# Kernel tuning notes

Measured on AMD Instinct MI355X. Metric: run time of the kernel, lower is better.

Reference implementation:

```python
import math
import jax, jax.numpy as jnp
import numpy as np

B, D, C = 1024, 512, 100000
S = 30.0
M = 0.3
COS_M = math.cos(M)
SIN_M = math.sin(M)
TH = math.cos(math.pi - M)
MM = math.sin(math.pi - M) * M
EPS = 1e-12  # torch F.normalize eps


def _l2norm(x):
    n = jnp.sqrt(jnp.sum(x * x, axis=-1, keepdims=True))
    return x / jnp.maximum(n, EPS)


def setup_inputs() -> dict:
    key = jax.random.key(0)
    k1, k2, k3 = jax.random.split(key, 3)
    features = jax.random.normal(k1, (B, D), dtype=jnp.float32)
    # xavier_uniform_ for weight [C, D]
    limit = math.sqrt(6.0 / (C + D))
    weight = jax.random.uniform(k2, (C, D), dtype=jnp.float32, minval=-limit, maxval=limit)
    targets = jax.random.randint(k3, (B,), 0, C, dtype=jnp.int64)
    return {"features": features, "weight": weight, "targets": targets}


def reference(features, weight, targets):
    # cosine similarity via normalized GEMM: [B, C]
    cosine = _l2norm(features) @ _l2norm(weight).T
    cosine = cosine.astype(jnp.float32)
    sine = jnp.sqrt(jnp.maximum(1.0 - cosine * cosine, 0.0))
    phi = cosine * COS_M - sine * SIN_M
    # easy_margin=False branch
    phi = jnp.where(cosine > TH, phi, cosine - MM)
    # one-hot blend (ls_eps == 0): target column gets phi, rest keep cosine
    one_hot = targets[:, None] == jnp.arange(C)[None, :]
    logits = jnp.where(one_hot, phi, cosine) * S
    # CrossEntropyLoss (mean reduction)
    logp = jax.nn.log_softmax(logits, axis=-1)
    loss = -jnp.mean(jnp.take_along_axis(logp, targets[:, None], axis=1))
    return loss
```

## Files before the change

### kernel.cpp

```cpp
#include <hip/hip_runtime.h>

#define B_ROWS 1024
#define D_DIM  512
#define C_CLS  100000
#define N_TILES 782
#define GRID_NJ 98

typedef unsigned short u16;
typedef __attribute__((ext_vector_type(8))) short bf16x8;
typedef __attribute__((ext_vector_type(4))) float f32x4;

__device__ __forceinline__ u16 f2bf(float f) {
  unsigned u = __float_as_uint(f);
  u += 0x7fffu + ((u >> 16) & 1u);
  return (u16)(u >> 16);
}

__device__ __forceinline__ bf16x8 pack8(float4 a, float4 b) {
  union { bf16x8 v; unsigned u[4]; } r;
  r.u[0] = __builtin_amdgcn_perm(__float_as_uint(a.y), __float_as_uint(a.x), 0x07060302u);
  r.u[1] = __builtin_amdgcn_perm(__float_as_uint(a.w), __float_as_uint(a.z), 0x07060302u);
  r.u[2] = __builtin_amdgcn_perm(__float_as_uint(b.y), __float_as_uint(b.x), 0x07060302u);
  r.u[3] = __builtin_amdgcn_perm(__float_as_uint(b.w), __float_as_uint(b.z), 0x07060302u);
  return r.v;
}

__device__ __forceinline__ void gll16(const void* g, void* l) {
  __builtin_amdgcn_global_load_lds(
      (const __attribute__((address_space(1))) unsigned int*)g,
      (__attribute__((address_space(3))) unsigned int*)l, 16, 0, 0);
}

__global__ void norm_feat_kernel(const float* __restrict__ in, u16* __restrict__ out)
{
  const int row  = blockIdx.x * 4 + (threadIdx.x >> 6);
  const int lane = threadIdx.x & 63;
  const float4* r = (const float4*)(in + (size_t)row * D_DIM);
  float4 v0 = r[lane];
  float4 v1 = r[lane + 64];
  float ss = v0.x*v0.x + v0.y*v0.y + v0.z*v0.z + v0.w*v0.w
           + v1.x*v1.x + v1.y*v1.y + v1.z*v1.z + v1.w*v1.w;
#pragma unroll
  for (int m = 1; m < 64; m <<= 1) ss += __shfl_xor(ss, m);
  const float inv = 1.0f / fmaxf(sqrtf(ss), 1e-12f);
  ushort4 o0, o1;
  o0.x = f2bf(v0.x * inv); o0.y = f2bf(v0.y * inv);
  o0.z = f2bf(v0.z * inv); o0.w = f2bf(v0.w * inv);
  o1.x = f2bf(v1.x * inv); o1.y = f2bf(v1.y * inv);
  o1.z = f2bf(v1.z * inv); o1.w = f2bf(v1.w * inv);
  ushort4* orow = (ushort4*)(out + (size_t)row * D_DIM);
  orow[lane]      = o0;
  orow[lane + 64] = o1;
}

__global__ __launch_bounds__(256, 4) void arc_gemm(
    const u16* __restrict__ fn, const float* __restrict__ wt,
    const int* __restrict__ targets, float* __restrict__ psum,
    float* __restrict__ tlogit)
{
  __shared__ u16 As[128 * 32];
  __shared__ u16 Ws[128 * 32];
  __shared__ int tg[128];
  __shared__ float winv[128];

  const int tid = threadIdx.x;
  const int bx  = blockIdx.x;
  const int xcd = bx & 7;
  const int l   = bx >> 3;
  const int tile_ni = (l >> 3) * 8 + xcd;
  if (tile_ni >= N_TILES) return;
  const int tile_m = (l & 7) << 7;
  const int tile_n = tile_ni << 7;

  if (tid < 128) tg[tid] = targets[tile_m + tid];

  const int wave = tid >> 6, lane = tid & 63;
  const int wm = wave >> 1, wno = wave & 1;
  const int quad = lane >> 4, l15 = lane & 15;

  f32x4 acc[4][4] = {};

  const int srow   = tid >> 2;
  const int schunk = (tid & 3) ^ ((tid >> 3) & 3);
  const u16* Ag = fn + (size_t)(tile_m + srow) * D_DIM + schunk * 8;
  u16* Asd0 = As + tid * 8;
  u16* Asd1 = As + 2048 + tid * 8;
  const int wr0 = tile_n + srow;
  const int wr1 = wr0 + 64;
  const float* Wg0 = wt + (size_t)min(wr0, C_CLS - 1) * D_DIM + schunk * 8;
  const float* Wg1 = wt + (size_t)min(wr1, C_CLS - 1) * D_DIM + schunk * 8;
  u16* Wsd0 = Ws + tid * 8;
  u16* Wsd1 = Ws + 2048 + tid * 8;

  const int rsw = (quad ^ ((l15 >> 1) & 3)) * 8;
  const u16* ApA = As + (wm * 64 + l15) * 32 + rsw;
  const u16* ApW = Ws + (wno * 64 + l15) * 32 + rsw;

  float ssq0 = 0.0f, ssq1 = 0.0f;

  for (int k0 = 0; k0 < D_DIM; k0 += 32) {
    const float4 wa = *(const float4*)(Wg0 + k0);
    const float4 wb = *(const float4*)(Wg0 + k0 + 4);
    const float4 wc = *(const float4*)(Wg1 + k0);
    const float4 wd = *(const float4*)(Wg1 + k0 + 4);
    gll16(Ag + k0, Asd0);
    gll16(Ag + 64 * D_DIM + k0, Asd1);
    ssq0 += wa.x*wa.x + wa.y*wa.y + wa.z*wa.z + wa.w*wa.w
          + wb.x*wb.x + wb.y*wb.y + wb.z*wb.z + wb.w*wb.w;
    ssq1 += wc.x*wc.x + wc.y*wc.y + wc.z*wc.z + wc.w*wc.w
          + wd.x*wd.x + wd.y*wd.y + wd.z*wd.z + wd.w*wd.w;
    *(bf16x8*)Wsd0 = pack8(wa, wb);
    *(bf16x8*)Wsd1 = pack8(wc, wd);
    __syncthreads();
    bf16x8 af[4], wf[4];
#pragma unroll
    for (int r = 0; r < 4; r++) af[r] = *(const bf16x8*)(ApA + r * 16 * 32);
#pragma unroll
    for (int r = 0; r < 4; r++) wf[r] = *(const bf16x8*)(ApW + r * 16 * 32);
#pragma unroll
    for (int rm = 0; rm < 4; rm++)
#pragma unroll
      for (int rn = 0; rn < 4; rn++)
        acc[rm][rn] = __builtin_amdgcn_mfma_f32_16x16x32_bf16(
            af[rm], wf[rn], acc[rm][rn], 0, 0, 0);
    __syncthreads();
  }

  ssq0 += __shfl_xor(ssq0, 1); ssq0 += __shfl_xor(ssq0, 2);
  ssq1 += __shfl_xor(ssq1, 1); ssq1 += __shfl_xor(ssq1, 2);
  if ((tid & 3) == 0) {
    winv[srow]      = 1.0f / fmaxf(sqrtf(ssq0), 1e-12f);
    winv[srow + 64] = 1.0f / fmaxf(sqrtf(ssq1), 1e-12f);
  }
  __syncthreads();

  float wiv[4];
#pragma unroll
  for (int rn = 0; rn < 4; rn++) wiv[rn] = winv[wno * 64 + rn * 16 + l15];

  const float Sc   = 30.0f;
  const float COSM = 0.9553364891256060f;
  const float SINM = 0.2955202066613396f;
  const float THc  = -0.9553364891256060f;
  const float MMc  = 0.0886560619984019f;

#pragma unroll
  for (int rm = 0; rm < 4; rm++) {
#pragma unroll
    for (int reg = 0; reg < 4; reg++) {
      const int bl = wm * 64 + rm * 16 + quad * 4 + reg;
      const int b = tile_m + bl;
      const int tgt = tg[bl];
      float s = 0.0f;
#pragma unroll
      for (int rn = 0; rn < 4; rn++) {
        const int c = tile_n + wno * 64 + rn * 16 + l15;
        const float cosv = acc[rm][rn][reg] * wiv[rn];
        float logit = Sc * cosv;
        if (c == tgt) {
          const float sine = sqrtf(fmaxf(1.0f - cosv * cosv, 0.0f));
          float phi = cosv * COSM - sine * SINM;
          phi = (cosv > THc) ? phi : (cosv - MMc);
          logit = Sc * phi;
          tlogit[b] = logit;
        }
        s += (c < C_CLS) ? __expf(logit - 30.0f) : 0.0f;
      }
      s += __shfl_xor(s, 1);
      s += __shfl_xor(s, 2);
      s += __shfl_xor(s, 4);
      s += __shfl_xor(s, 8);
      if (l15 == 0) atomicAdd(psum + b, s);
    }
  }
}

__global__ void finalize_loss(const float* __restrict__ psum,
                              const float* __restrict__ tlogit,
                              float* __restrict__ out)
{
  const int tid = threadIdx.x;
  float s = 0.0f;
  for (int i = tid; i < B_ROWS; i += 256)
    s += 30.0f + logf(psum[i]) - tlogit[i];
#pragma unroll
  for (int m = 1; m < 64; m <<= 1) s += __shfl_xor(s, m);
  __shared__ float red[4];
  if ((tid & 63) == 0) red[tid >> 6] = s;
  __syncthreads();
  if (tid == 0) out[0] = (red[0] + red[1] + red[2] + red[3]) * (1.0f / B_ROWS);
}

extern "C" void kernel_launch(void* const* d_in, const int* in_sizes, int n_in,
                              void* d_out, int out_size, void* d_ws, size_t ws_size,
                              hipStream_t stream) {
  const float* feat = (const float*)d_in[0];
  const float* wt   = (const float*)d_in[1];
  const int*   tgt  = (const int*)d_in[2];
  float* out = (float*)d_out;
  char* ws = (char*)d_ws;

  u16* fn = (u16*)ws;
  float* psum = (float*)(ws + (size_t)B_ROWS * D_DIM * 2);
  float* tlogit = psum + B_ROWS;

  hipMemsetAsync(psum, 0, B_ROWS * sizeof(float), stream);
  norm_feat_kernel<<<B_ROWS / 4, 256, 0, stream>>>(feat, fn);
  arc_gemm<<<GRID_NJ * 8 * 8, 256, 0, stream>>>(fn, wt, tgt, psum, tlogit);
  finalize_loss<<<1, 256, 0, stream>>>(psum, tlogit, out);
}
```

Before: 460.5 us.

## Load GEMM operands directly into registers with double buffering, dropping LDS staging

Removes the shared-memory tiles and block barriers from the ArcFace GEMM. Each lane now loads its own MFMA fragments of features and weights straight from global memory into registers, double-buffered across k-steps, and computes weight norms with cross-lane shuffles. The goal is to eliminate LDS traffic and __syncthreads stalls. The cost is redundant global loads, since each weight row is fetched by both wm waves and each feature row by both wno waves. Register pressure also rises, so launch bounds drop occupancy from 4 to 2 blocks.

```diff
diff --git a/kernel.cpp b/kernel.cpp
--- a/kernel.cpp
+++ b/kernel.cpp
@@ -25,12 +25,6 @@
   return r.v;
 }
 
-__device__ __forceinline__ void gll16(const void* g, void* l) {
-  __builtin_amdgcn_global_load_lds(
-      (const __attribute__((address_space(1))) unsigned int*)g,
-      (__attribute__((address_space(3))) unsigned int*)l, 16, 0, 0);
-}
-
 __global__ void norm_feat_kernel(const float* __restrict__ in, u16* __restrict__ out)
 {
   const int row  = blockIdx.x * 4 + (threadIdx.x >> 6);
@@ -53,16 +47,11 @@
   orow[lane + 64] = o1;
 }
 
-__global__ __launch_bounds__(256, 4) void arc_gemm(
+__global__ __launch_bounds__(256, 2) void arc_gemm(
     const u16* __restrict__ fn, const float* __restrict__ wt,
     const int* __restrict__ targets, float* __restrict__ psum,
     float* __restrict__ tlogit)
 {
-  __shared__ u16 As[128 * 32];
-  __shared__ u16 Ws[128 * 32];
-  __shared__ int tg[128];
-  __shared__ float winv[128];
-
   const int tid = threadIdx.x;
   const int bx  = blockIdx.x;
   const int xcd = bx & 7;
@@ -72,71 +61,68 @@
   const int tile_m = (l & 7) << 7;
   const int tile_n = tile_ni << 7;
 
-  if (tid < 128) tg[tid] = targets[tile_m + tid];
-
   const int wave = tid >> 6, lane = tid & 63;
   const int wm = wave >> 1, wno = wave & 1;
   const int quad = lane >> 4, l15 = lane & 15;
 
+  const u16*   Ab[4];
+  const float* Wb[4];
+#pragma unroll
+  for (int r = 0; r < 4; r++) {
+    Ab[r] = fn + (size_t)(tile_m + wm * 64 + r * 16 + l15) * D_DIM + quad * 8;
+    const int wr = tile_n + wno * 64 + r * 16 + l15;
+    Wb[r] = wt + (size_t)min(wr, C_CLS - 1) * D_DIM + quad * 8;
+  }
+
   f32x4 acc[4][4] = {};
+  float ssq[4] = {0.f, 0.f, 0.f, 0.f};
 
-  const int srow   = tid >> 2;
-  const int schunk = (tid & 3) ^ ((tid >> 3) & 3);
-  const u16* Ag = fn + (size_t)(tile_m + srow) * D_DIM + schunk * 8;
-  u16* Asd0 = As + tid * 8;
-  u16* Asd1 = As + 2048 + tid * 8;
-  const int wr0 = tile_n + srow;
-  const int wr1 = wr0 + 64;
-  const float* Wg0 = wt + (size_t)min(wr0, C_CLS - 1) * D_DIM + schunk * 8;
-  const float* Wg1 = wt + (size_t)min(wr1, C_CLS - 1) * D_DIM + schunk * 8;
-  u16* Wsd0 = Ws + tid * 8;
-  u16* Wsd1 = Ws + 2048 + tid * 8;
+  bf16x8 a[2][4];
+  float4 w[2][4][2];
 
-  const int rsw = (quad ^ ((l15 >> 1) & 3)) * 8;
-  const u16* ApA = As + (wm * 64 + l15) * 32 + rsw;
-  const u16* ApW = Ws + (wno * 64 + l15) * 32 + rsw;
+#pragma unroll
+  for (int r = 0; r < 4; r++) {
+    a[0][r]    = *(const bf16x8*)(Ab[r]);
+    w[0][r][0] = *(const float4*)(Wb[r]);
+    w[0][r][1] = *(const float4*)(Wb[r] + 4);
+  }
 
-  float ssq0 = 0.0f, ssq1 = 0.0f;
-
-  for (int k0 = 0; k0 < D_DIM; k0 += 32) {
-    const float4 wa = *(const float4*)(Wg0 + k0);
-    const float4 wb = *(const float4*)(Wg0 + k0 + 4);
-    const float4 wc = *(const float4*)(Wg1 + k0);
-    const float4 wd = *(const float4*)(Wg1 + k0 + 4);
-    gll16(Ag + k0, Asd0);
-    gll16(Ag + 64 * D_DIM + k0, Asd1);
-    ssq0 += wa.x*wa.x + wa.y*wa.y + wa.z*wa.z + wa.w*wa.w
-          + wb.x*wb.x + wb.y*wb.y + wb.z*wb.z + wb.w*wb.w;
-    ssq1 += wc.x*wc.x + wc.y*wc.y + wc.z*wc.z + wc.w*wc.w
-          + wd.x*wd.x + wd.y*wd.y + wd.z*wd.z + wd.w*wd.w;
-    *(bf16x8*)Wsd0 = pack8(wa, wb);
-    *(bf16x8*)Wsd1 = pack8(wc, wd);
-    __syncthreads();
-    bf16x8 af[4], wf[4];
 #pragma unroll
-    for (int r = 0; r < 4; r++) af[r] = *(const bf16x8*)(ApA + r * 16 * 32);
+  for (int i = 0; i < 16; ++i) {
+    const int cur = i & 1, nxt = cur ^ 1;
+    if (i < 15) {
+      const int k0 = (i + 1) * 32;
 #pragma unroll
-    for (int r = 0; r < 4; r++) wf[r] = *(const bf16x8*)(ApW + r * 16 * 32);
+      for (int r = 0; r < 4; r++) {
+        a[nxt][r]    = *(const bf16x8*)(Ab[r] + k0);
+        w[nxt][r][0] = *(const float4*)(Wb[r] + k0);
+        w[nxt][r][1] = *(const float4*)(Wb[r] + k0 + 4);
+      }
+    }
+    bf16x8 wf[4];
+#pragma unroll
+    for (int r = 0; r < 4; r++) {
+      const float4 x = w[cur][r][0], y = w[cur][r][1];
+      ssq[r] += x.x*x.x + x.y*x.y + x.z*x.z + x.w*x.w
+              + y.x*y.x + y.y*y.y + y.z*y.z + y.w*y.w;
+      wf[r] = pack8(x, y);
+    }
 #pragma unroll
     for (int rm = 0; rm < 4; rm++)
 #pragma unroll
       for (int rn = 0; rn < 4; rn++)
         acc[rm][rn] = __builtin_amdgcn_mfma_f32_16x16x32_bf16(
-            af[rm], wf[rn], acc[rm][rn], 0, 0, 0);
-    __syncthreads();
+            a[cur][rm], wf[rn], acc[rm][rn], 0, 0, 0);
   }
-
-  ssq0 += __shfl_xor(ssq0, 1); ssq0 += __shfl_xor(ssq0, 2);
-  ssq1 += __shfl_xor(ssq1, 1); ssq1 += __shfl_xor(ssq1, 2);
-  if ((tid & 3) == 0) {
-    winv[srow]      = 1.0f / fmaxf(sqrtf(ssq0), 1e-12f);
-    winv[srow + 64] = 1.0f / fmaxf(sqrtf(ssq1), 1e-12f);
-  }
-  __syncthreads();
 
   float wiv[4];
 #pragma unroll
-  for (int rn = 0; rn < 4; rn++) wiv[rn] = winv[wno * 64 + rn * 16 + l15];
+  for (int r = 0; r < 4; r++) {
+    float s = ssq[r];
+    s += __shfl_xor(s, 16);
+    s += __shfl_xor(s, 32);
+    wiv[r] = 1.0f / fmaxf(sqrtf(s), 1e-12f);
+  }
 
   const float Sc   = 30.0f;
   const float COSM = 0.9553364891256060f;
@@ -150,7 +136,7 @@
     for (int reg = 0; reg < 4; reg++) {
       const int bl = wm * 64 + rm * 16 + quad * 4 + reg;
       const int b = tile_m + bl;
-      const int tgt = tg[bl];
+      const int tgt = targets[b];
       float s = 0.0f;
 #pragma unroll
       for (int rn = 0; rn < 4; rn++) {
```

Measured after the change: 783.3 us. 1.7x slower.

## Double-buffer LDS tiles and prefetch next K-slice during MFMA compute

Applied to the files above, without the earlier changes.

Converts the GEMM main loop to a two-stage software pipeline. Shared A/W tiles are double-buffered and fully unrolled, so the loads for the next K step (global_load_lds for features, fp32 weight loads) are issued before the current step's MFMAs, and one barrier per iteration is removed. The bf16 conversion and LDS store of the weights happen after the MFMAs. Target indices are now read straight from global memory in the epilogue instead of being staged in shared memory. This doubles LDS use and raises register pressure, which may hurt occupancy at 4 blocks per CU.

```diff
diff --git a/kernel.cpp b/kernel.cpp
--- a/kernel.cpp
+++ b/kernel.cpp
@@ -58,9 +58,8 @@
     const int* __restrict__ targets, float* __restrict__ psum,
     float* __restrict__ tlogit)
 {
-  __shared__ u16 As[128 * 32];
-  __shared__ u16 Ws[128 * 32];
-  __shared__ int tg[128];
+  __shared__ u16 As[2][4096];
+  __shared__ u16 Ws[2][4096];
   __shared__ float winv[128];
 
   const int tid = threadIdx.x;
@@ -72,8 +71,6 @@
   const int tile_m = (l & 7) << 7;
   const int tile_n = tile_ni << 7;
 
-  if (tid < 128) tg[tid] = targets[tile_m + tid];
-
   const int wave = tid >> 6, lane = tid & 63;
   const int wm = wave >> 1, wno = wave & 1;
   const int quad = lane >> 4, l15 = lane & 15;
@@ -83,47 +80,66 @@
   const int srow   = tid >> 2;
   const int schunk = (tid & 3) ^ ((tid >> 3) & 3);
   const u16* Ag = fn + (size_t)(tile_m + srow) * D_DIM + schunk * 8;
-  u16* Asd0 = As + tid * 8;
-  u16* Asd1 = As + 2048 + tid * 8;
   const int wr0 = tile_n + srow;
-  const int wr1 = wr0 + 64;
   const float* Wg0 = wt + (size_t)min(wr0, C_CLS - 1) * D_DIM + schunk * 8;
-  const float* Wg1 = wt + (size_t)min(wr1, C_CLS - 1) * D_DIM + schunk * 8;
-  u16* Wsd0 = Ws + tid * 8;
-  u16* Wsd1 = Ws + 2048 + tid * 8;
+  const float* Wg1 = wt + (size_t)min(wr0 + 64, C_CLS - 1) * D_DIM + schunk * 8;
+  const int ldst = tid * 8;
 
   const int rsw = (quad ^ ((l15 >> 1) & 3)) * 8;
-  const u16* ApA = As + (wm * 64 + l15) * 32 + rsw;
-  const u16* ApW = Ws + (wno * 64 + l15) * 32 + rsw;
+  const int ra  = (wm * 64 + l15) * 32 + rsw;
+  const int rw  = (wno * 64 + l15) * 32 + rsw;
 
   float ssq0 = 0.0f, ssq1 = 0.0f;
 
-  for (int k0 = 0; k0 < D_DIM; k0 += 32) {
-    const float4 wa = *(const float4*)(Wg0 + k0);
-    const float4 wb = *(const float4*)(Wg0 + k0 + 4);
-    const float4 wc = *(const float4*)(Wg1 + k0);
-    const float4 wd = *(const float4*)(Wg1 + k0 + 4);
-    gll16(Ag + k0, Asd0);
-    gll16(Ag + 64 * D_DIM + k0, Asd1);
+  gll16(Ag,              &As[0][ldst]);
+  gll16(Ag + 64 * D_DIM, &As[0][2048 + ldst]);
+  {
+    const float4 wa = *(const float4*)(Wg0);
+    const float4 wb = *(const float4*)(Wg0 + 4);
+    const float4 wc = *(const float4*)(Wg1);
+    const float4 wd = *(const float4*)(Wg1 + 4);
     ssq0 += wa.x*wa.x + wa.y*wa.y + wa.z*wa.z + wa.w*wa.w
           + wb.x*wb.x + wb.y*wb.y + wb.z*wb.z + wb.w*wb.w;
     ssq1 += wc.x*wc.x + wc.y*wc.y + wc.z*wc.z + wc.w*wc.w
           + wd.x*wd.x + wd.y*wd.y + wd.z*wd.z + wd.w*wd.w;
-    *(bf16x8*)Wsd0 = pack8(wa, wb);
-    *(bf16x8*)Wsd1 = pack8(wc, wd);
+    *(bf16x8*)&Ws[0][ldst]        = pack8(wa, wb);
+    *(bf16x8*)&Ws[0][2048 + ldst] = pack8(wc, wd);
+  }
+
+#pragma unroll
+  for (int i = 0; i < 16; ++i) {
     __syncthreads();
+    float4 wa, wb, wc, wd;
+    const int nb = (i + 1) & 1;
+    if (i < 15) {
+      const int kn = (i + 1) * 32;
+      gll16(Ag + kn,              &As[nb][ldst]);
+      gll16(Ag + 64 * D_DIM + kn, &As[nb][2048 + ldst]);
+      wa = *(const float4*)(Wg0 + kn);
+      wb = *(const float4*)(Wg0 + kn + 4);
+      wc = *(const float4*)(Wg1 + kn);
+      wd = *(const float4*)(Wg1 + kn + 4);
+    }
+    const int cb = i & 1;
     bf16x8 af[4], wf[4];
 #pragma unroll
-    for (int r = 0; r < 4; r++) af[r] = *(const bf16x8*)(ApA + r * 16 * 32);
-#pragma unroll
-    for (int r = 0; r < 4; r++) wf[r] = *(const bf16x8*)(ApW + r * 16 * 32);
+    for (int r = 0; r < 4; r++) af[r] = *(const bf16x8*)&As[cb][ra + r * 16 * 32];
+#pragma unroll
+    for (int r = 0; r < 4; r++) wf[r] = *(const bf16x8*)&Ws[cb][rw + r * 16 * 32];
 #pragma unroll
     for (int rm = 0; rm < 4; rm++)
 #pragma unroll
       for (int rn = 0; rn < 4; rn++)
         acc[rm][rn] = __builtin_amdgcn_mfma_f32_16x16x32_bf16(
             af[rm], wf[rn], acc[rm][rn], 0, 0, 0);
-    __syncthreads();
+    if (i < 15) {
+      ssq0 += wa.x*wa.x + wa.y*wa.y + wa.z*wa.z + wa.w*wa.w
+            + wb.x*wb.x + wb.y*wb.y + wb.z*wb.z + wb.w*wb.w;
+      ssq1 += wc.x*wc.x + wc.y*wc.y + wc.z*wc.z + wc.w*wc.w
+            + wd.x*wd.x + wd.y*wd.y + wd.z*wd.z + wd.w*wd.w;
+      *(bf16x8*)&Ws[nb][ldst]        = pack8(wa, wb);
+      *(bf16x8*)&Ws[nb][2048 + ldst] = pack8(wc, wd);
+    }
   }
 
   ssq0 += __shfl_xor(ssq0, 1); ssq0 += __shfl_xor(ssq0, 2);
@@ -150,7 +166,7 @@
     for (int reg = 0; reg < 4; reg++) {
       const int bl = wm * 64 + rm * 16 + quad * 4 + reg;
       const int b = tile_m + bl;
-      const int tgt = tg[bl];
+      const int tgt = targets[b];
       float s = 0.0f;
 #pragma unroll
       for (int rn = 0; rn < 4; rn++) {
```

New measurement: 508.5 us. 1.1x slower.
